# Kernel optimization log

Hardware: AMD Instinct MI355X
Metric: run time of the kernel (lower is better)

The kernel has to match this reference:

```python
import jax, jax.numpy as jnp
import numpy as np
import math

B, S = 4, 1024
N_ITEMS, EMB = 50000, 128
H, D = 4, 32


def setup_inputs() -> dict:
    key = jax.random.key(0)
    ks = jax.random.split(key, 12)

    def lin(k, fan_in, fan_out):
        lim = 1.0 / math.sqrt(fan_in)
        return jax.random.uniform(k, (fan_in, fan_out), minval=-lim, maxval=lim, dtype=jnp.float32)

    inp = {}
    inp["sequence_item_indices"] = jax.random.randint(ks[0], (B, S), 0, N_ITEMS, dtype=jnp.int32)
    inp["sequence_correct_flags"] = jax.random.randint(ks[1], (B, S), 0, 2, dtype=jnp.int32)
    inp["sequence_time_gaps"] = jax.random.uniform(ks[2], (B, S), dtype=jnp.float32) * 100.0
    inp["item_emb"] = jax.random.normal(ks[3], (N_ITEMS, EMB), dtype=jnp.float32) * 0.02
    inp["ans_emb"] = jax.random.normal(ks[4], (2, EMB), dtype=jnp.float32) * 0.02
    inp["Wq"] = lin(ks[5], EMB, H * D); inp["bq"] = jnp.zeros((H * D,), jnp.float32)
    inp["Wk"] = lin(ks[6], EMB, H * D); inp["bk"] = jnp.zeros((H * D,), jnp.float32)
    inp["Wv"] = lin(ks[7], EMB, H * D); inp["bv"] = jnp.zeros((H * D,), jnp.float32)
    inp["Wh"] = lin(ks[8], 2 * EMB, EMB); inp["bh"] = jnp.zeros((EMB,), jnp.float32)
    inp["W1"] = lin(ks[9], H * D + EMB, EMB); inp["b1"] = jnp.zeros((EMB,), jnp.float32)
    inp["W2"] = lin(ks[10], EMB, 1); inp["b2"] = jnp.zeros((1,), jnp.float32)
    inp["theta_raw"] = jnp.zeros((H,), jnp.float32)
    return inp


def reference(sequence_item_indices, sequence_correct_flags, sequence_time_gaps,
              item_emb, ans_emb, Wq, bq, Wk, bk, Wv, bv, Wh, bh, W1, b1, W2, b2, theta_raw):
    Bb, Ss = sequence_item_indices.shape
    Hn = theta_raw.shape[0]
    Dd = Wq.shape[1] // Hn

    e = item_emb[sequence_item_indices]                      # [B,S,E]
    a = ans_emb[sequence_correct_flags]                      # [B,S,E]
    inter = jnp.concatenate([e, a], axis=-1) @ Wh + bh       # history_projection

    Q = (e @ Wq + bq).reshape(Bb, Ss, Hn, Dd)
    K = (e @ Wk + bk).reshape(Bb, Ss, Hn, Dd)
    V = (inter @ Wv + bv).reshape(Bb, Ss, Hn, Dd)
    scale = 1.0 / jnp.sqrt(jnp.float32(Dd))

    # self relevance per history position; per-target softmax over i<t done via exclusive prefix sums
    sr = jnp.sum(Q * K, axis=-1) * scale                     # [B,S,H]
    ex = jnp.exp(sr - jnp.max(sr, axis=1, keepdims=True))    # shift-invariant
    Ep = jnp.concatenate([jnp.zeros((Bb, 1, Hn), sr.dtype), jnp.cumsum(ex, axis=1)], axis=1)  # [B,S+1,H]

    g = jnp.maximum(sequence_time_gaps.astype(jnp.float32), 1.0)
    Pp = jnp.concatenate([jnp.zeros((Bb, 1), g.dtype), jnp.cumsum(g, axis=1)], axis=1)        # [B,S+1]

    t = jnp.arange(1, Ss)                                    # targets, T = S-1
    i = jnp.arange(Ss)                                       # history positions
    mask = i[None, :] < t[:, None]                           # [T,S]
    step = (t[:, None] - i[None, :]).astype(jnp.float32)     # arange(L,0,-1)[i] == t - i
    gap_diff = Pp[:, 1:Ss, None] - Pp[:, None, :Ss]          # [B,T,S]  sum_{j in [i,t)} clamp(gap,1)
    Et = Ep[:, 1:Ss, :]                                      # [B,T,H]  softmax normalizer Z_t
    rel = (Et[:, :, None, :] - Ep[:, None, :Ss, :]) / Et[:, :, None, :]  # cumulative relevance [B,T,S,H]
    pd = jnp.where(mask[None, :, :, None],
                   step[None, :, :, None] * gap_diff[..., None] * rel, 0.0)  # perceived distance

    theta = jax.nn.softplus(theta_raw) + 1e-4                # [H]
    decay = jnp.exp(-theta * pd)                             # [B,T,S,H]

    # candidate query at position t equals query_projection(item_embedding[t])
    raw = jnp.einsum('bthd,bihd->btih', Q[:, 1:], K) * scale # [B,T,S,H]
    scores = jnp.where(mask[None, :, :, None], raw * decay, -1e30)
    attn = jax.nn.softmax(scores, axis=2)                    # softmax over history positions
    ctx = jnp.einsum('btih,bihd->bthd', attn, V).reshape(Bb, Ss - 1, Hn * Dd)

    feat = jnp.concatenate([ctx, e[:, 1:]], axis=-1)
    h1 = jax.nn.relu(feat @ W1 + b1)                         # dropout is inference identity
    logit = (h1 @ W2 + b2)[..., 0]
    pred = jax.nn.sigmoid(logit)                             # [B,S-1]
    valid = jnp.ones((Bb, Ss - 1), dtype=bool)               # all positions valid (no padding)
    return pred, valid
```

## Files before the change

### kernel.cpp

```cpp
#include <hip/hip_runtime.h>
#include <math.h>

#define BSZ 4
#define SSZ 1024
#define EMBD 128
#define HN 4
#define DN 32
#define TQ (SSZ - 1)
#define NROWS (BSZ * TQ)

typedef __attribute__((ext_vector_type(8))) short bf16x8;
typedef __attribute__((ext_vector_type(4))) short bf16x4;
typedef __attribute__((ext_vector_type(4))) float f32x4;

static __device__ __forceinline__ unsigned short f2bf(float x) {
    union { float f; unsigned u; } v; v.f = x;
    unsigned r = v.u + 0x7fffu + ((v.u >> 16) & 1u);
    return (unsigned short)(r >> 16);
}
static __device__ __forceinline__ bf16x8 cvt8(const float4 a, const float4 b) {
    bf16x8 v;
    v[0] = (short)f2bf(a.x); v[1] = (short)f2bf(a.y);
    v[2] = (short)f2bf(a.z); v[3] = (short)f2bf(a.w);
    v[4] = (short)f2bf(b.x); v[5] = (short)f2bf(b.y);
    v[6] = (short)f2bf(b.z); v[7] = (short)f2bf(b.w);
    return v;
}

__global__ __launch_bounds__(256)
void embed4_kernel(const int* __restrict__ idx, const int* __restrict__ flg,
                   const float* __restrict__ item_emb, const float* __restrict__ ans_emb,
                   const float* __restrict__ Wq, const float* __restrict__ bq,
                   const float* __restrict__ Wk, const float* __restrict__ bk,
                   const float* __restrict__ Wv, const float* __restrict__ bv,
                   const float* __restrict__ Wh, const float* __restrict__ bh_bias,
                   unsigned short* __restrict__ Qts, unsigned short* __restrict__ Kts,
                   unsigned short* __restrict__ Vts,
                   float* __restrict__ ec, float* __restrict__ srw)
{
    __shared__ __align__(16) unsigned short esb[16][136];
    __shared__ __align__(16) unsigned short asb[16][136];
    __shared__ __align__(16) unsigned short intb[16][136];
    __shared__ __align__(16) unsigned short Wt[128][40];

    const int tid = threadIdx.x;
    const int tok0 = blockIdx.x * 16;
    const int b = blockIdx.x >> 6;
    const int s0 = tok0 & 1023;
    const int w = tid >> 6, lane = tid & 63;
    const int quad = lane >> 4, col = lane & 15;

    {
        const int tk = tid >> 4;
        const int d0 = (tid & 15) * 8;
        const int tok = tok0 + tk;
        const float* esrc = item_emb + (size_t)idx[tok] * EMBD + d0;
        const float* asrc = ans_emb + (size_t)flg[tok] * EMBD + d0;
        const float4 e0 = *(const float4*)esrc;
        const float4 e1 = *(const float4*)(esrc + 4);
        const float4 a0 = *(const float4*)asrc;
        const float4 a1 = *(const float4*)(asrc + 4);
        *(float4*)(ec + (size_t)tok * EMBD + d0) = e0;
        *(float4*)(ec + (size_t)tok * EMBD + d0 + 4) = e1;
        *(bf16x8*)&esb[tk][d0] = cvt8(e0, e1);
        *(bf16x8*)&asb[tk][d0] = cvt8(a0, a1);
    }

    const int jb = (tid & 31) * 4;
    const int ib = (tid >> 5) * 4;
    float rr[4][4];

    #define WSRC(R) ((R) < 8 ? Wh + (size_t)(R) * 4096                     \
                  : (R) < 12 ? Wq + (size_t)((R) - 8) * 4096               \
                  : (R) < 16 ? Wk + (size_t)((R) - 12) * 4096              \
                  : Wv + (size_t)((R) - 16) * 4096)
    #define LOADW(P)                                                       \
    {                                                                      \
        const float* _p = (P);                                             \
        *(float4*)rr[0] = *(const float4*)(_p + (ib + 0) * 128 + jb);      \
        *(float4*)rr[1] = *(const float4*)(_p + (ib + 1) * 128 + jb);      \
        *(float4*)rr[2] = *(const float4*)(_p + (ib + 2) * 128 + jb);      \
        *(float4*)rr[3] = *(const float4*)(_p + (ib + 3) * 128 + jb);      \
    }
    #define STOREW                                                         \
    {                                                                      \
        _Pragma("unroll")                                                  \
        for (int jj = 0; jj < 4; jj++) {                                   \
            bf16x4 v;                                                      \
            v[0] = (short)f2bf(rr[0][jj]); v[1] = (short)f2bf(rr[1][jj]);  \
            v[2] = (short)f2bf(rr[2][jj]); v[3] = (short)f2bf(rr[3][jj]);  \
            *(bf16x4*)&Wt[jb + jj][ib] = v;                                \
        }                                                                  \
    }

    f32x4 accI[2] = {{0.f,0.f,0.f,0.f},{0.f,0.f,0.f,0.f}};
    f32x4 accQ[2] = {{0.f,0.f,0.f,0.f},{0.f,0.f,0.f,0.f}};
    f32x4 accK[2] = {{0.f,0.f,0.f,0.f},{0.f,0.f,0.f,0.f}};
    f32x4 accV[2] = {{0.f,0.f,0.f,0.f},{0.f,0.f,0.f,0.f}};

    LOADW(WSRC(0));
    #pragma unroll
    for (int r = 0; r < 20; r++) {
        __syncthreads();
        STOREW;
        __syncthreads();
        if (r < 19) LOADW(WSRC(r + 1));

        const unsigned short (*Ab)[136] = (r < 4) ? esb : (r < 8) ? asb
                                        : (r < 16) ? esb : intb;
        const int koff = ((r < 8) ? (r & 3) : (r < 12) ? (r - 8)
                        : (r < 16) ? (r - 12) : (r - 16)) * 32;
        const bf16x8 af = *(const bf16x8*)&Ab[col][koff + quad * 8];
        f32x4* acc = (r < 8) ? accI : (r < 12) ? accQ : (r < 16) ? accK : accV;
        #pragma unroll
        for (int ntl = 0; ntl < 2; ntl++) {
            const bf16x8 bf = *(const bf16x8*)&Wt[w * 32 + ntl * 16 + col][quad * 8];
            acc[ntl] = __builtin_amdgcn_mfma_f32_16x16x32_bf16(af, bf, acc[ntl], 0, 0, 0);
        }
        if (r == 7) {
            #pragma unroll
            for (int ntl = 0; ntl < 2; ntl++) {
                const int j = w * 32 + ntl * 16 + col;
                const float bb = bh_bias[j];
                #pragma unroll
                for (int r4 = 0; r4 < 4; r4++)
                    intb[quad * 4 + r4][j] = f2bf(accI[ntl][r4] + bb);
            }
        }
    }
    #undef LOADW
    #undef STOREW
    #undef WSRC

    const int bhn = b * HN + w;
    const float scale = 0.17677669529663687f;
    float p[4] = {0.f, 0.f, 0.f, 0.f};
    #pragma unroll
    for (int ntl = 0; ntl < 2; ntl++) {
        const int j = w * 32 + ntl * 16 + col;
        const float bQ = bq[j], bK = bk[j], bV = bv[j];
        #pragma unroll
        for (int r = 0; r < 4; r++) {
            const float qv = accQ[ntl][r] + bQ;
            const float kv = accK[ntl][r] + bK;
            const int s = s0 + quad * 4 + r;
            const size_t o = ((size_t)bhn * SSZ + s) * DN + ntl * 16 + col;
            Qts[o] = f2bf(qv * scale);
            Kts[o] = f2bf(kv);
            Vts[o] = f2bf(accV[ntl][r] + bV);
            p[r] = fmaf(qv, kv, p[r]);
        }
    }
    #pragma unroll
    for (int r = 0; r < 4; r++) {
        float pr = p[r];
        pr += __shfl_xor(pr, 1, 64);
        pr += __shfl_xor(pr, 2, 64);
        pr += __shfl_xor(pr, 4, 64);
        pr += __shfl_xor(pr, 8, 64);
        if (col == 0)
            srw[(size_t)bhn * SSZ + s0 + quad * 4 + r] = pr * scale;
    }
}

__global__ __launch_bounds__(256)
void attn4_kernel(const unsigned short* __restrict__ Qts,
                  const unsigned short* __restrict__ Kts,
                  const unsigned short* __restrict__ Vts,
                  const float* __restrict__ srw, const float* __restrict__ gaps,
                  const float* __restrict__ theta_raw, float* __restrict__ csw,
                  float* __restrict__ ls)
{
    __shared__ __align__(16) unsigned short Ks[64][40];
    __shared__ __align__(16) unsigned short Vs[32][72];
    __shared__ __align__(16) unsigned short Ps[4][16][72];
    __shared__ float EpS[SSZ + 1];
    __shared__ float PpS[SSZ + 1];
    __shared__ float wtot[4];

    const int bid = blockIdx.x;
    const int qr = bid & 3;
    const int qt = (bid >> 2) & 15;
    const int bh = bid >> 6;
    const int b = bh >> 2, h = bh & 3;
    const int tid = threadIdx.x;
    const int w = tid >> 6, lane = tid & 63;
    const int quad = lane >> 4, col = lane & 15;
    const int t0 = qt * 64 + 1;

    const int nc = qt + 1;
    const int c0r = (nc * qr) >> 2;
    const int c1r = (nc * (qr + 1)) >> 2;

    {
        const float4 sv = *(const float4*)(srw + (size_t)bh * SSZ + tid * 4);
        const float e0 = __expf(sv.x);
        const float p0 = e0;
        const float p1 = p0 + __expf(sv.y);
        const float p2 = p1 + __expf(sv.z);
        const float p3 = p2 + __expf(sv.w);
        float s = p3;
        #pragma unroll
        for (int d = 1; d < 64; d <<= 1) {
            const float t = __shfl_up(s, d, 64);
            if (lane >= d) s += t;
        }
        if (lane == 63) wtot[w] = s;
        __syncthreads();
        float base = s - p3;
        for (int ww = 0; ww < w; ww++) base += wtot[ww];
        EpS[tid * 4 + 1] = base + p0;
        EpS[tid * 4 + 2] = base + p1;
        EpS[tid * 4 + 3] = base + p2;
        EpS[tid * 4 + 4] = base + p3;
        if (tid == 0) EpS[0] = 0.0f;
    }
    {
        const float4 gv = *(const float4*)(gaps + (size_t)b * SSZ + tid * 4);
        const float p0 = fmaxf(gv.x, 1.0f);
        const float p1 = p0 + fmaxf(gv.y, 1.0f);
        const float p2 = p1 + fmaxf(gv.z, 1.0f);
        const float p3 = p2 + fmaxf(gv.w, 1.0f);
        float s = p3;
        #pragma unroll
        for (int d = 1; d < 64; d <<= 1) {
            const float t = __shfl_up(s, d, 64);
            if (lane >= d) s += t;
        }
        __syncthreads();
        if (lane == 63) wtot[w] = s;
        __syncthreads();
        float base = s - p3;
        for (int ww = 0; ww < w; ww++) base += wtot[ww];
        PpS[tid * 4 + 1] = base + p0;
        PpS[tid * 4 + 2] = base + p1;
        PpS[tid * 4 + 3] = base + p2;
        PpS[tid * 4 + 4] = base + p3;
        if (tid == 0) PpS[0] = 0.0f;
    }
    __syncthreads();

    const float theta = logf(1.0f + __expf(theta_raw[h])) + 1e-4f;
    const float nth = -theta;
    float Ept[4], Ppt[4], iEp[4], tft[4];
    int qrow[4], tq[4];
    #pragma unroll
    for (int r = 0; r < 4; r++) {
        qrow[r] = w * 16 + quad * 4 + r;
        tq[r] = t0 + qrow[r];
        tft[r] = (float)tq[r];
        Ept[r] = EpS[tq[r]];
        Ppt[r] = PpS[tq[r]];
        iEp[r] = 1.0f / Ept[r];
    }

    bf16x8 aq;
    {
        int t = t0 + w * 16 + col; if (t > 1023) t = 1023;
        aq = *(const bf16x8*)(Qts + ((size_t)(bh * SSZ + t)) * DN + quad * 8);
    }

    f32x4 acc0 = {0.f, 0.f, 0.f, 0.f};
    f32x4 acc1 = {0.f, 0.f, 0.f, 0.f};
    float lsum[4] = {0.f, 0.f, 0.f, 0.f};

    const int i_st = tid >> 2;
    const int d0 = (tid & 3) * 8;
    bf16x8 kreg = *(const bf16x8*)(Kts + ((size_t)(bh * SSZ + c0r * 64 + i_st)) * DN + d0);
    bf16x8 vreg = *(const bf16x8*)(Vts + ((size_t)(bh * SSZ + c0r * 64 + i_st)) * DN + d0);

    for (int c = c0r; c < c1r; c++) {
        __syncthreads();
        *(bf16x8*)&Ks[i_st][d0] = kreg;
        #pragma unroll
        for (int k2 = 0; k2 < 8; k2++) Vs[d0 + k2][i_st] = (unsigned short)vreg[k2];
        __syncthreads();
        if (c + 1 < c1r) {
            const size_t o = ((size_t)(bh * SSZ + (c + 1) * 64 + i_st)) * DN + d0;
            kreg = *(const bf16x8*)(Kts + o);
            vreg = *(const bf16x8*)(Vts + o);
        }

        const bool full = (c < qt);
        #pragma unroll
        for (int nt = 0; nt < 4; nt++) {
            const bf16x8 bk = *(const bf16x8*)&Ks[nt * 16 + col][quad * 8];
            f32x4 z = {0.f, 0.f, 0.f, 0.f};
            f32x4 raw = __builtin_amdgcn_mfma_f32_16x16x32_bf16(aq, bk, z, 0, 0, 0);
            const int il = nt * 16 + col;
            const int i_ = c * 64 + il;
            const float Epi = EpS[i_];
            const float Ppi = PpS[i_];
            const float fi = (float)i_;
            #pragma unroll
            for (int r = 0; r < 4; r++) {
                const float pdv = (tft[r] - fi) * (Ppt[r] - Ppi) * ((Ept[r] - Epi) * iEp[r]);
                const float sc  = raw[r] * __expf(nth * pdv);
                float p = __expf(sc);
                p = (full || il <= qrow[r]) ? p : 0.0f;
                lsum[r] += p;
                Ps[w][quad * 4 + r][il] = f2bf(p);
            }
        }
        #pragma unroll
        for (int ks = 0; ks < 2; ks++) {
            const bf16x8 ap = *(const bf16x8*)&Ps[w][col][ks * 32 + quad * 8];
            const bf16x8 bv0 = *(const bf16x8*)&Vs[col][ks * 32 + quad * 8];
            const bf16x8 bv1 = *(const bf16x8*)&Vs[16 + col][ks * 32 + quad * 8];
            acc0 = __builtin_amdgcn_mfma_f32_16x16x32_bf16(ap, bv0, acc0, 0, 0, 0);
            acc1 = __builtin_amdgcn_mfma_f32_16x16x32_bf16(ap, bv1, acc1, 0, 0, 0);
        }
    }

    #pragma unroll
    for (int r = 0; r < 4; r++) {
        float lr = lsum[r];
        #pragma unroll
        for (int msk = 8; msk >= 1; msk >>= 1) lr += __shfl_xor(lr, msk, 64);
        lsum[r] = lr;
    }
    const size_t cswh = (size_t)qr * NROWS * EMBD;
    const size_t lsh  = (size_t)qr * (HN * BSZ * SSZ) + ((size_t)bh << 10);
    #pragma unroll
    for (int r = 0; r < 4; r++) {
        if (tq[r] <= 1023) {
            float* dst = csw + cswh + ((size_t)(b * TQ + (tq[r] - 1))) * EMBD + h * DN;
            dst[col]      = acc0[r];
            dst[16 + col] = acc1[r];
            if (col == 0) ls[lsh + tq[r]] = lsum[r];
        }
    }
}

__global__ __launch_bounds__(256)
void mlp3_kernel(const float* __restrict__ csw, const float* __restrict__ ls,
                 const float* __restrict__ ec,
                 const float* __restrict__ W1, const float* __restrict__ b1,
                 const float* __restrict__ W2, const float* __restrict__ b2,
                 float* __restrict__ out)
{
    __shared__ __align__(16) unsigned short featb[32][264];
    __shared__ __align__(16) unsigned short W1t[128][264];
    __shared__ float sred[4][16];

    const int tid = threadIdx.x;
    const int r0 = blockIdx.x * 32;
    const int w = tid >> 6, lane = tid & 63;
    const int quad = lane >> 4, col = lane & 15;
    const int mt = w & 1, nh = w >> 1;

    {
        const int jb = (tid & 31) * 4;
        const int ib = (tid >> 5) * 4;
        for (int ic = 0; ic < 8; ic++) {
            const int i0 = ic * 32 + ib;
            float rr[4][4];
            *(float4*)rr[0] = *(const float4*)(W1 + (size_t)(i0 + 0) * 128 + jb);
            *(float4*)rr[1] = *(const float4*)(W1 + (size_t)(i0 + 1) * 128 + jb);
            *(float4*)rr[2] = *(const float4*)(W1 + (size_t)(i0 + 2) * 128 + jb);
            *(float4*)rr[3] = *(const float4*)(W1 + (size_t)(i0 + 3) * 128 + jb);
            #pragma unroll
            for (int jj = 0; jj < 4; jj++) {
                bf16x4 v;
                v[0] = (short)f2bf(rr[0][jj]); v[1] = (short)f2bf(rr[1][jj]);
                v[2] = (short)f2bf(rr[2][jj]); v[3] = (short)f2bf(rr[3][jj]);
                *(bf16x4*)&W1t[jb + jj][i0] = v;
            }
        }
    }
    {
        const int rr = tid >> 3;
        const int c0 = (tid & 7) * 32;
        int row = r0 + rr; if (row >= NROWS) row = NROWS - 1;
        if (c0 < 128) {
            const int bb = row / TQ;
            const int tt = row - bb * TQ + 1;
            const int hh = c0 >> 5;
            const size_t LSS = (size_t)HN * BSZ * SSZ;
            const size_t CSS = (size_t)NROWS * EMBD;
            const size_t lsi = ((size_t)(bb * HN + hh) << 10) + tt;
            const float lt = ls[lsi] + ls[LSS + lsi] + ls[2 * LSS + lsi]
                           + ls[3 * LSS + lsi];
            const float inv = 1.0f / lt;
            const size_t base = (size_t)row * EMBD + c0;
            #pragma unroll
            for (int g = 0; g < 4; g++) {
                float4 f0 = ((const float4*)(csw + base))[g * 2];
                float4 f1 = ((const float4*)(csw + base))[g * 2 + 1];
                #pragma unroll
                for (int q = 1; q < 4; q++) {
                    const float4 g0 = ((const float4*)(csw + q * CSS + base))[g * 2];
                    const float4 g1 = ((const float4*)(csw + q * CSS + base))[g * 2 + 1];
                    f0.x += g0.x; f0.y += g0.y; f0.z += g0.z; f0.w += g0.w;
                    f1.x += g1.x; f1.y += g1.y; f1.z += g1.z; f1.w += g1.w;
                }
                f0.x *= inv; f0.y *= inv; f0.z *= inv; f0.w *= inv;
                f1.x *= inv; f1.y *= inv; f1.z *= inv; f1.w *= inv;
                *(bf16x8*)&featb[rr][c0 + g * 8] = cvt8(f0, f1);
            }
        } else {
            const int bb = row / TQ;
            const int tt = row - bb * TQ + 1;
            const float* src = ec + ((size_t)(bb * SSZ + tt)) * EMBD + (c0 - 128);
            #pragma unroll
            for (int g = 0; g < 4; g++) {
                const float4 f0 = ((const float4*)src)[g * 2];
                const float4 f1 = ((const float4*)src)[g * 2 + 1];
                *(bf16x8*)&featb[rr][c0 + g * 8] = cvt8(f0, f1);
            }
        }
    }
    __syncthreads();

    float s[4] = {0.f, 0.f, 0.f, 0.f};
    #pragma unroll
    for (int ntl = 0; ntl < 4; ntl++) {
        const int nt = nh * 4 + ntl;
        f32x4 acc = {0.f, 0.f, 0.f, 0.f};
        #pragma unroll
        for (int kc = 0; kc < 8; kc++) {
            const bf16x8 af = *(const bf16x8*)&featb[mt * 16 + col][kc * 32 + quad * 8];
            const bf16x8 bf = *(const bf16x8*)&W1t[nt * 16 + col][kc * 32 + quad * 8];
            acc = __builtin_amdgcn_mfma_f32_16x16x32_bf16(af, bf, acc, 0, 0, 0);
        }
        const int j = nt * 16 + col;
        const float b1j = b1[j], w2j = W2[j];
        #pragma unroll
        for (int r = 0; r < 4; r++)
            s[r] = fmaf(fmaxf(acc[r] + b1j, 0.0f), w2j, s[r]);
    }
    #pragma unroll
    for (int r = 0; r < 4; r++) {
        float sr = s[r];
        sr += __shfl_xor(sr, 1, 64);
        sr += __shfl_xor(sr, 2, 64);
        sr += __shfl_xor(sr, 4, 64);
        sr += __shfl_xor(sr, 8, 64);
        if (col == 0) sred[w][quad * 4 + r] = sr;
    }
    __syncthreads();
    if (tid < 32) {
        const int mt2 = tid >> 4, rr = tid & 15;
        const float logit = sred[mt2][rr] + sred[mt2 + 2][rr] + b2[0];
        const int grow = r0 + tid;
        if (grow < NROWS) {
            out[grow] = 1.0f / (1.0f + __expf(-logit));
            out[NROWS + grow] = 1.0f;
        }
    }
}

extern "C" void kernel_launch(void* const* d_in, const int* in_sizes, int n_in,
                              void* d_out, int out_size, void* d_ws, size_t ws_size,
                              hipStream_t stream)
{
    const int*   idx       = (const int*)d_in[0];
    const int*   flg       = (const int*)d_in[1];
    const float* gaps      = (const float*)d_in[2];
    const float* item_emb  = (const float*)d_in[3];
    const float* ans_emb   = (const float*)d_in[4];
    const float* Wq        = (const float*)d_in[5];
    const float* bq        = (const float*)d_in[6];
    const float* Wk        = (const float*)d_in[7];
    const float* bk        = (const float*)d_in[8];
    const float* Wv        = (const float*)d_in[9];
    const float* bv        = (const float*)d_in[10];
    const float* Wh        = (const float*)d_in[11];
    const float* bh        = (const float*)d_in[12];
    const float* W1        = (const float*)d_in[13];
    const float* b1        = (const float*)d_in[14];
    const float* W2        = (const float*)d_in[15];
    const float* b2        = (const float*)d_in[16];
    const float* theta_raw = (const float*)d_in[17];
    (void)in_sizes; (void)n_in; (void)ws_size;

    const size_t QKV = (size_t)BSZ * HN * SSZ * DN;
    unsigned short* Qts = (unsigned short*)d_ws;
    unsigned short* Kts = Qts + QKV;
    unsigned short* Vts = Kts + QKV;
    float* ec  = (float*)(Vts + QKV);
    float* srw = ec + (size_t)BSZ * SSZ * EMBD;
    float* csw = srw + (size_t)BSZ * HN * SSZ;
    float* ls  = csw + 4 * (size_t)NROWS * EMBD;

    float* out = (float*)d_out;

    embed4_kernel<<<BSZ * SSZ / 16, 256, 0, stream>>>(
        idx, flg, item_emb, ans_emb, Wq, bq, Wk, bk, Wv, bv, Wh, bh,
        Qts, Kts, Vts, ec, srw);
    attn4_kernel<<<BSZ * HN * 64, 256, 0, stream>>>(
        Qts, Kts, Vts, srw, gaps, theta_raw, csw, ls);
    mlp3_kernel<<<(NROWS + 31) / 32, 256, 0, stream>>>(
        csw, ls, ec, W1, b1, W2, b2, out);
}
```

Measured before the change: 145.3 us.

## Hoist prefix-sum scans into a separate kernel and stream per-chunk slices

The exp/gap prefix scans were redone by all 1024 attention blocks. They now run once in a small scan kernel that writes the scans to global workspace. The attention kernel loads only the 64-element slice it needs per chunk into shared memory, prefetched alongside K/V. This cuts redundant work and shared memory use (possibly raising occupancy), at the cost of an extra kernel launch and a global round trip.

```diff
diff --git a/kernel.cpp b/kernel.cpp
--- a/kernel.cpp
+++ b/kernel.cpp
@@ -8,6 +8,7 @@
 #define DN 32
 #define TQ (SSZ - 1)
 #define NROWS (BSZ * TQ)
+#define EPSTRIDE 1088
 
 typedef __attribute__((ext_vector_type(8))) short bf16x8;
 typedef __attribute__((ext_vector_type(4))) short bf16x4;
@@ -164,19 +165,61 @@
 }
 
 __global__ __launch_bounds__(256)
-void attn4_kernel(const unsigned short* __restrict__ Qts,
+void scan0_kernel(const float* __restrict__ srw, const float* __restrict__ gaps,
+                  float* __restrict__ EpG, float* __restrict__ PpG)
+{
+    __shared__ float wtot[4];
+    const int tid = threadIdx.x;
+    const int w = tid >> 6, lane = tid & 63;
+    const int bid = blockIdx.x;
+
+    float p0, p1, p2, p3;
+    float* dst;
+    if (bid < 16) {
+        const float4 sv = *(const float4*)(srw + (size_t)bid * SSZ + tid * 4);
+        p0 = __expf(sv.x);
+        p1 = p0 + __expf(sv.y);
+        p2 = p1 + __expf(sv.z);
+        p3 = p2 + __expf(sv.w);
+        dst = EpG + (size_t)bid * EPSTRIDE;
+    } else {
+        const float4 gv = *(const float4*)(gaps + (size_t)(bid - 16) * SSZ + tid * 4);
+        p0 = fmaxf(gv.x, 1.0f);
+        p1 = p0 + fmaxf(gv.y, 1.0f);
+        p2 = p1 + fmaxf(gv.z, 1.0f);
+        p3 = p2 + fmaxf(gv.w, 1.0f);
+        dst = PpG + (size_t)(bid - 16) * EPSTRIDE;
+    }
+    float s = p3;
+    #pragma unroll
+    for (int d = 1; d < 64; d <<= 1) {
+        const float t = __shfl_up(s, d, 64);
+        if (lane >= d) s += t;
+    }
+    if (lane == 63) wtot[w] = s;
+    __syncthreads();
+    float base = s - p3;
+    for (int ww = 0; ww < w; ww++) base += wtot[ww];
+    dst[tid * 4 + 1] = base + p0;
+    dst[tid * 4 + 2] = base + p1;
+    dst[tid * 4 + 3] = base + p2;
+    dst[tid * 4 + 4] = base + p3;
+    if (tid == 0) dst[0] = 0.0f;
+}
+
+__global__ __launch_bounds__(256)
+void attn5_kernel(const unsigned short* __restrict__ Qts,
                   const unsigned short* __restrict__ Kts,
                   const unsigned short* __restrict__ Vts,
-                  const float* __restrict__ srw, const float* __restrict__ gaps,
+                  const float* __restrict__ EpG, const float* __restrict__ PpG,
                   const float* __restrict__ theta_raw, float* __restrict__ csw,
                   float* __restrict__ ls)
 {
     __shared__ __align__(16) unsigned short Ks[64][40];
     __shared__ __align__(16) unsigned short Vs[32][72];
     __shared__ __align__(16) unsigned short Ps[4][16][72];
-    __shared__ float EpS[SSZ + 1];
-    __shared__ float PpS[SSZ + 1];
-    __shared__ float wtot[4];
+    __shared__ float EpL[64];
+    __shared__ float PpL[64];
 
     const int bid = blockIdx.x;
     const int qr = bid & 3;
@@ -192,53 +235,8 @@
     const int c0r = (nc * qr) >> 2;
     const int c1r = (nc * (qr + 1)) >> 2;
 
-    {
-        const float4 sv = *(const float4*)(srw + (size_t)bh * SSZ + tid * 4);
-        const float e0 = __expf(sv.x);
-        const float p0 = e0;
-        const float p1 = p0 + __expf(sv.y);
-        const float p2 = p1 + __expf(sv.z);
-        const float p3 = p2 + __expf(sv.w);
-        float s = p3;
-        #pragma unroll
-        for (int d = 1; d < 64; d <<= 1) {
-            const float t = __shfl_up(s, d, 64);
-            if (lane >= d) s += t;
-        }
-        if (lane == 63) wtot[w] = s;
-        __syncthreads();
-        float base = s - p3;
-        for (int ww = 0; ww < w; ww++) base += wtot[ww];
-        EpS[tid * 4 + 1] = base + p0;
-        EpS[tid * 4 + 2] = base + p1;
-        EpS[tid * 4 + 3] = base + p2;
-        EpS[tid * 4 + 4] = base + p3;
-        if (tid == 0) EpS[0] = 0.0f;
-    }
-    {
-        const float4 gv = *(const float4*)(gaps + (size_t)b * SSZ + tid * 4);
-        const float p0 = fmaxf(gv.x, 1.0f);
-        const float p1 = p0 + fmaxf(gv.y, 1.0f);
-        const float p2 = p1 + fmaxf(gv.z, 1.0f);
-        const float p3 = p2 + fmaxf(gv.w, 1.0f);
-        float s = p3;
-        #pragma unroll
-        for (int d = 1; d < 64; d <<= 1) {
-            const float t = __shfl_up(s, d, 64);
-            if (lane >= d) s += t;
-        }
-        __syncthreads();
-        if (lane == 63) wtot[w] = s;
-        __syncthreads();
-        float base = s - p3;
-        for (int ww = 0; ww < w; ww++) base += wtot[ww];
-        PpS[tid * 4 + 1] = base + p0;
-        PpS[tid * 4 + 2] = base + p1;
-        PpS[tid * 4 + 3] = base + p2;
-        PpS[tid * 4 + 4] = base + p3;
-        if (tid == 0) PpS[0] = 0.0f;
-    }
-    __syncthreads();
+    const float* Eprow = EpG + (size_t)bh * EPSTRIDE;
+    const float* Pprow = PpG + (size_t)b * EPSTRIDE;
 
     const float theta = logf(1.0f + __expf(theta_raw[h])) + 1e-4f;
     const float nth = -theta;
@@ -249,8 +247,8 @@
         qrow[r] = w * 16 + quad * 4 + r;
         tq[r] = t0 + qrow[r];
         tft[r] = (float)tq[r];
-        Ept[r] = EpS[tq[r]];
-        Ppt[r] = PpS[tq[r]];
+        Ept[r] = Eprow[tq[r]];
+        Ppt[r] = Pprow[tq[r]];
         iEp[r] = 1.0f / Ept[r];
     }
 
@@ -268,17 +266,24 @@
     const int d0 = (tid & 3) * 8;
     bf16x8 kreg = *(const bf16x8*)(Kts + ((size_t)(bh * SSZ + c0r * 64 + i_st)) * DN + d0);
     bf16x8 vreg = *(const bf16x8*)(Vts + ((size_t)(bh * SSZ + c0r * 64 + i_st)) * DN + d0);
+    float spre = 0.0f;
+    if (tid < 64)       spre = Eprow[c0r * 64 + tid];
+    else if (tid < 128) spre = Pprow[c0r * 64 + (tid - 64)];
 
     for (int c = c0r; c < c1r; c++) {
         __syncthreads();
         *(bf16x8*)&Ks[i_st][d0] = kreg;
         #pragma unroll
         for (int k2 = 0; k2 < 8; k2++) Vs[d0 + k2][i_st] = (unsigned short)vreg[k2];
+        if (tid < 64)       EpL[tid] = spre;
+        else if (tid < 128) PpL[tid - 64] = spre;
         __syncthreads();
         if (c + 1 < c1r) {
             const size_t o = ((size_t)(bh * SSZ + (c + 1) * 64 + i_st)) * DN + d0;
             kreg = *(const bf16x8*)(Kts + o);
             vreg = *(const bf16x8*)(Vts + o);
+            if (tid < 64)       spre = Eprow[(c + 1) * 64 + tid];
+            else if (tid < 128) spre = Pprow[(c + 1) * 64 + (tid - 64)];
         }
 
         const bool full = (c < qt);
@@ -288,10 +293,9 @@
             f32x4 z = {0.f, 0.f, 0.f, 0.f};
             f32x4 raw = __builtin_amdgcn_mfma_f32_16x16x32_bf16(aq, bk, z, 0, 0, 0);
             const int il = nt * 16 + col;
-            const int i_ = c * 64 + il;
-            const float Epi = EpS[i_];
-            const float Ppi = PpS[i_];
-            const float fi = (float)i_;
+            const float Epi = EpL[il];
+            const float Ppi = PpL[il];
+            const float fi = (float)(c * 64 + il);
             #pragma unroll
             for (int r = 0; r < 4; r++) {
                 const float pdv = (tft[r] - fi) * (Ppt[r] - Ppi) * ((Ept[r] - Epi) * iEp[r]);
@@ -482,14 +486,17 @@
     float* srw = ec + (size_t)BSZ * SSZ * EMBD;
     float* csw = srw + (size_t)BSZ * HN * SSZ;
     float* ls  = csw + 4 * (size_t)NROWS * EMBD;
+    float* EpG = ls + 4 * (size_t)HN * BSZ * SSZ;
+    float* PpG = EpG + 16 * (size_t)EPSTRIDE;
 
     float* out = (float*)d_out;
 
     embed4_kernel<<<BSZ * SSZ / 16, 256, 0, stream>>>(
         idx, flg, item_emb, ans_emb, Wq, bq, Wk, bk, Wv, bv, Wh, bh,
         Qts, Kts, Vts, ec, srw);
-    attn4_kernel<<<BSZ * HN * 64, 256, 0, stream>>>(
-        Qts, Kts, Vts, srw, gaps, theta_raw, csw, ls);
+    scan0_kernel<<<20, 256, 0, stream>>>(srw, gaps, EpG, PpG);
+    attn5_kernel<<<BSZ * HN * 64, 256, 0, stream>>>(
+        Qts, Kts, Vts, EpG, PpG, theta_raw, csw, ls);
     mlp3_kernel<<<(NROWS + 31) / 32, 256, 0, stream>>>(
         csw, ls, ec, W1, b1, W2, b2, out);
 }
```

Result: no change. 146.4 us (+0.8%).
